# Kernel optimization log

Hardware: AMD Instinct MI355X
Metric: run time of the kernel (lower is better)

The kernel has to match this reference:

```python
import jax, jax.numpy as jnp
import numpy as np
from jax import lax

EPS_LN = 1e-5
EPS_NORM = 1e-12

def conv1x1(x, w):
    # x: [b,c,h,w], w: [o,c]
    return jnp.einsum('oc,bchw->bohw', w, x)

def dwconv3x3(x, w):
    # depthwise 3x3, w: [c,1,3,3]
    return lax.conv_general_dilated(
        x, w, window_strides=(1, 1), padding=[(1, 1), (1, 1)],
        feature_group_count=x.shape[1],
        dimension_numbers=('NCHW', 'OIHW', 'NCHW'))

def layernorm_chan(x, w, b):
    # WithBias LayerNorm over channel dim of NCHW (torch does it in b,(hw),c layout)
    mu = jnp.mean(x, axis=1, keepdims=True)
    var = jnp.mean((x - mu) ** 2, axis=1, keepdims=True)
    xn = (x - mu) / jnp.sqrt(var + EPS_LN)
    return xn * w[None, :, None, None] + b[None, :, None, None]

def l2norm(x):
    n = jnp.sqrt(jnp.sum(x * x, axis=-1, keepdims=True))
    return x / jnp.maximum(n, EPS_NORM)

def setup_inputs() -> dict:
    key = jax.random.key(0)
    ks = jax.random.split(key, 8)
    dim, heads, hidden = 64, 2, 170
    b, h, w = 2, 256, 256
    s = 0.05
    return {
        'x': jax.random.normal(ks[0], (b, dim, h, w), jnp.float32),
        'ln1_w': jnp.ones((dim,), jnp.float32),
        'ln1_b': jnp.zeros((dim,), jnp.float32),
        'w_qkv': jax.random.normal(ks[1], (dim * 3, dim), jnp.float32) * s,
        'dw_qkv': jax.random.normal(ks[2], (dim * 3, 1, 3, 3), jnp.float32) * s,
        'temperature': jnp.ones((heads, 1, 1), jnp.float32),
        'w_po': jax.random.normal(ks[3], (dim, dim), jnp.float32) * s,
        'ln2_w': jnp.ones((dim,), jnp.float32),
        'ln2_b': jnp.zeros((dim,), jnp.float32),
        'w_in': jax.random.normal(ks[4], (hidden * 2, dim), jnp.float32) * s,
        'dw_ffn': jax.random.normal(ks[5], (hidden * 2, 1, 3, 3), jnp.float32) * s,
        'w_out': jax.random.normal(ks[6], (dim, hidden), jnp.float32) * s,
    }

def attention(x, w_qkv, dw_qkv, temperature, w_po, num_heads):
    b, c, h, w = x.shape
    qkv = dwconv3x3(conv1x1(x, w_qkv), dw_qkv)            # [b,3c,h,w]
    q, k, v = jnp.split(qkv, 3, axis=1)
    def heads(t):
        return t.reshape(b, num_heads, c // num_heads, h * w)  # [b,hd,ch,hw]
    q, k, v = heads(q), heads(k), heads(v)
    q = l2norm(q)
    k = l2norm(k)
    attn = jnp.einsum('bhcs,bhds->bhcd', q, k) * temperature[None]  # [b,hd,ch,ch]
    attn = jax.nn.softmax(attn, axis=-1)
    out = jnp.einsum('bhcd,bhds->bhcs', attn, v)
    out = out.reshape(b, c, h, w)
    return conv1x1(out, w_po)

def gdfn(x, w_in, dw_ffn, w_out):
    x = dwconv3x3(conv1x1(x, w_in), dw_ffn)
    x1, x2 = jnp.split(x, 2, axis=1)
    return conv1x1(jax.nn.gelu(x1, approximate=False) * x2, w_out)

def reference(x, ln1_w, ln1_b, w_qkv, dw_qkv, temperature, w_po,
              ln2_w, ln2_b, w_in, dw_ffn, w_out):
    num_heads = temperature.shape[0]
    x = x + attention(layernorm_chan(x, ln1_w, ln1_b), w_qkv, dw_qkv,
                      temperature, w_po, num_heads)
    x = x + gdfn(layernorm_chan(x, ln2_w, ln2_b), w_in, dw_ffn, w_out)
    return x
```

## Files before the change

kernel.cpp:

```cpp
#include <hip/hip_runtime.h>
#include <math.h>

#define HW 65536

typedef __attribute__((ext_vector_type(8))) short short8;
typedef __attribute__((ext_vector_type(4))) float floatx4;
typedef __attribute__((ext_vector_type(4))) unsigned short ushortx4;

__device__ __forceinline__ float bf2f(unsigned short u){
  unsigned v = ((unsigned)u)<<16; float f; __builtin_memcpy(&f,&v,4); return f;
}
__device__ __forceinline__ unsigned short f2bf(float f){
  unsigned u; __builtin_memcpy(&u,&f,4);
  u += 0x7fffu + ((u>>16)&1u);
  return (unsigned short)(u>>16);
}
__device__ __forceinline__ int is_f32(const void* magic){
  return ((const unsigned*)magic)[0] == 0x3F800000u;
}
__device__ __forceinline__ float ldv(const void* p, size_t i, int f32){
  return f32 ? ((const float*)p)[i] : bf2f(((const unsigned short*)p)[i]);
}

__global__ __launch_bounds__(64) void k_fold(const void* __restrict__ w_qkv,
                       const void* __restrict__ ln1_w,
                       const void* __restrict__ ln1_b,
                       const void* __restrict__ w_in,
                       const void* __restrict__ ln2_w,
                       const void* __restrict__ ln2_b,
                       const void* __restrict__ w_out,
                       unsigned short* __restrict__ A1, float* __restrict__ a1, float* __restrict__ b1,
                       unsigned short* __restrict__ A5, float* __restrict__ a5, float* __restrict__ b5,
                       unsigned short* __restrict__ A7){
  int f32 = is_f32(ln1_w);
  int bid = blockIdx.x; int c = threadIdx.x;
  if (bid < 192){
    int j = bid;
    float wv = ldv(w_qkv, j*64+c, f32);
    unsigned short q = f2bf(wv*ldv(ln1_w,c,f32));
    A1[j*64+c] = q;
    float sa = bf2f(q);
    float sb = wv*ldv(ln1_b,c,f32);
    #pragma unroll
    for(int o=1;o<64;o<<=1){ sa += __shfl_xor(sa,o,64); sb += __shfl_xor(sb,o,64); }
    if (c==0){ a1[j]=sa; b1[j]=sb; }
  } else if (bid < 576){
    int j = bid-192;
    float wv = (j<340)? ldv(w_in, j*64+c, f32) : 0.f;
    unsigned short q = f2bf(wv*ldv(ln2_w,c,f32));
    A5[j*64+c]=q;
    float sa = bf2f(q);
    float sb = wv*ldv(ln2_b,c,f32);
    #pragma unroll
    for(int o=1;o<64;o<<=1){ sa += __shfl_xor(sa,o,64); sb += __shfl_xor(sb,o,64); }
    if (c==0){ a5[j]=sa; b5[j]=sb; }
  } else {
    int j = bid-576;
    #pragma unroll
    for(int t=0;t<3;t++){
      int k=t*64+c;
      A7[j*192+k] = (k<170)? f2bf(ldv(w_out, j*170+k, f32)) : (unsigned short)0;
    }
  }
}

#define BTT_STR 72
template<int F32>
__device__ __forceinline__ void gemm_ln_body(
    const unsigned short* __restrict__ A, const void* __restrict__ Bv,
    const float* __restrict__ arow, const float* __restrict__ brow,
    unsigned short* __restrict__ out, int outC, int jmax, int ntiles)
{
  __shared__ unsigned short btt[64*BTT_STR];
  __shared__ float muL[64];
  __shared__ float rsL[64];
  int tid=threadIdx.x; int w=tid>>6, lane=tid&63, m=lane&15, quad=lane>>4;
  int sblk = blockIdx.x*64; int b=sblk>>16, s=sblk&65535;
  {
    int ch = lane, px0 = w*16;
    size_t src = (size_t)b*64*HW + (size_t)ch*HW + s + px0;
    unsigned short tmp[16];
    if (F32){
      const float* sp = (const float*)Bv + src;
      #pragma unroll
      for(int q4=0;q4<4;q4++){
        floatx4 fv = *(const floatx4*)(sp + q4*4);
        #pragma unroll
        for(int k=0;k<4;k++) tmp[q4*4+k] = f2bf(fv[k]);
      }
    } else {
      const unsigned short* sp = (const unsigned short*)Bv + src;
      short8 r0 = *(const short8*)sp;
      short8 r1 = *(const short8*)(sp+8);
      #pragma unroll
      for(int jj=0;jj<8;jj++){ tmp[jj]=(unsigned short)r0[jj]; tmp[8+jj]=(unsigned short)r1[jj]; }
    }
    #pragma unroll
    for(int jj=0;jj<16;jj++) btt[(px0+jj)*BTT_STR + ch] = tmp[jj];
  }
  __syncthreads();
  short8 bfr[4][2];
  #pragma unroll
  for(int st4=0; st4<4; st4++){
    const unsigned short* row = btt + (st4*16+m)*BTT_STR + quad*8;
    short8 v0 = *(const short8*)row;
    short8 v1 = *(const short8*)(row+32);
    bfr[st4][0]=v0; bfr[st4][1]=v1;
    float sm=0.f, sq=0.f;
    #pragma unroll
    for(int jj=0;jj<8;jj++){
      float a=bf2f((unsigned short)v0[jj]); sm+=a; sq+=a*a;
      float c=bf2f((unsigned short)v1[jj]); sm+=c; sq+=c*c;
    }
    sm += __shfl_xor(sm,16,64); sq += __shfl_xor(sq,16,64);
    sm += __shfl_xor(sm,32,64); sq += __shfl_xor(sq,32,64);
    float m_ = sm*(1.f/64.f);
    float var = sq*(1.f/64.f) - m_*m_;
    if (w==0 && quad==0){ muL[st4*16+m]=m_; rsL[st4*16+m]=1.f/sqrtf(var+1e-5f); }
  }
  __syncthreads();
  for(int jt=w; jt<ntiles; jt+=4){
    int j = jt*16 + m;
    const unsigned short* ap = A + j*64 + quad*8;
    short8 af0 = *(const short8*)ap;
    short8 af1 = *(const short8*)(ap+32);
    float aj = arow[j], bj = brow[j];
    unsigned short* op = out + ((size_t)b*outC + j)*HW + s;
    bool ok = (j < jmax);
    #pragma unroll
    for(int st4=0; st4<4; st4++){
      floatx4 acc = {0.f,0.f,0.f,0.f};
      acc = __builtin_amdgcn_mfma_f32_16x16x32_bf16(bfr[st4][0], af0, acc, 0,0,0);
      acc = __builtin_amdgcn_mfma_f32_16x16x32_bf16(bfr[st4][1], af1, acc, 0,0,0);
      floatx4 m4 = *(const floatx4*)(muL + st4*16 + quad*4);
      floatx4 r4 = *(const floatx4*)(rsL + st4*16 + quad*4);
      ushortx4 pk;
      #pragma unroll
      for(int r=0;r<4;r++) pk[r] = f2bf(r4[r]*(acc[r] - m4[r]*aj) + bj);
      if (ok) *(ushortx4*)(op + st4*16 + quad*4) = pk;
    }
  }
}
__global__ __launch_bounds__(256) void k_gemm_ln(
    const unsigned short* __restrict__ A, const void* __restrict__ B,
    const float* __restrict__ arow, const float* __restrict__ brow,
    unsigned short* __restrict__ out,
    int outC, int jmax, int ntiles, const void* __restrict__ magic, int mode)
{
  int f32 = (mode==1) ? 1 : (mode==2 ? 0 : is_f32(magic));
  if (f32) gemm_ln_body<1>(A,B,arow,brow,out,outC,jmax,ntiles);
  else     gemm_ln_body<0>(A,B,arow,brow,out,outC,jmax,ntiles);
}

#define GTT_STR 200
__global__ __launch_bounds__(256) void k_gemm_out(
    const unsigned short* __restrict__ A7, const unsigned short* __restrict__ G,
    const unsigned short* __restrict__ xmid, void* __restrict__ outp, const void* __restrict__ magic)
{
  __shared__ unsigned short gtt[64*GTT_STR];
  int f32 = is_f32(magic);
  int tid=threadIdx.x; int w=tid>>6, lane=tid&63, m=lane&15, quad=lane>>4;
  int sblk = blockIdx.x*64; int b=sblk>>16, s=sblk&65535;
  const unsigned short* Gb = G + (size_t)b*170*HW + s;
  {
    int px0 = w*16;
    #pragma unroll
    for(int rep=0; rep<3; rep++){
      int ch = rep*64 + lane;
      const unsigned short* sp = Gb + (size_t)ch*HW + px0;
      short8 r0 = *(const short8*)sp;
      short8 r1 = *(const short8*)(sp+8);
      #pragma unroll
      for(int jj=0;jj<8;jj++){
        gtt[(px0+jj)*GTT_STR + ch]   = (unsigned short)r0[jj];
        gtt[(px0+8+jj)*GTT_STR + ch] = (unsigned short)r1[jj];
      }
    }
  }
  __syncthreads();
  int j = w*16 + m;
  const unsigned short* ap = A7 + j*192 + quad*8;
  short8 af[6];
  #pragma unroll
  for(int ks=0;ks<6;ks++) af[ks] = *(const short8*)(ap + ks*32);
  #pragma unroll
  for(int st4=0; st4<4; st4++){
    const unsigned short* row = gtt + (st4*16+m)*GTT_STR + quad*8;
    floatx4 acc = {0.f,0.f,0.f,0.f};
    #pragma unroll
    for(int ks=0;ks<6;ks++){
      short8 bf = *(const short8*)(row + ks*32);
      acc = __builtin_amdgcn_mfma_f32_16x16x32_bf16(bf, af[ks], acc, 0,0,0);
    }
    size_t idx0 = ((size_t)b*64 + j)*HW + s + st4*16 + quad*4;
    ushortx4 xm4 = *(const ushortx4*)(xmid + idx0);
    if (f32){
      floatx4 o;
      #pragma unroll
      for(int r=0;r<4;r++) o[r] = acc[r] + bf2f(xm4[r]);
      *(floatx4*)((float*)outp + idx0) = o;
    } else {
      ushortx4 o;
      #pragma unroll
      for(int r=0;r<4;r++) o[r] = f2bf(acc[r] + bf2f(xm4[r]));
      *(ushortx4*)((unsigned short*)outp + idx0) = o;
    }
  }
}

__device__ __forceinline__ void load_row(const unsigned short* __restrict__ sp,
    int y, int x0, int oct, float* __restrict__ f){
  if((unsigned)y < 256u){
    const unsigned short* p = sp + y*256 + x0;
    short8 v = *(const short8*)p;
    #pragma unroll
    for(int k=0;k<8;k++) f[k+1] = bf2f((unsigned short)v[k]);
    f[0] = oct      ? bf2f(p[-1]) : 0.f;
    f[9] = (oct<31) ? bf2f(p[8])  : 0.f;
  } else {
    #pragma unroll
    for(int k=0;k<10;k++) f[k] = 0.f;
  }
}

__device__ __forceinline__ void conv_row(const float* __restrict__ r0,
    const float* __restrict__ r1, const float* __restrict__ r2,
    const float* __restrict__ w, float* __restrict__ o){
  #pragma unroll
  for(int k=0;k<8;k++){
    o[k] = w[0]*r0[k] + w[1]*r0[k+1] + w[2]*r0[k+2]
         + w[3]*r1[k] + w[4]*r1[k+1] + w[5]*r1[k+2]
         + w[6]*r2[k] + w[7]*r2[k+1] + w[8]*r2[k+2];
  }
}

__global__ __launch_bounds__(256) void k_dwconv(const unsigned short* __restrict__ src,
    const void* __restrict__ wdw, unsigned short* __restrict__ dst, int C,
    const void* __restrict__ magic){
  int f32 = is_f32(magic);
  int tid=threadIdx.x;
  int bc = blockIdx.y;
  int ch = bc % C;
  int oct = tid&31, strip = tid>>5;
  int x0 = oct*8;
  int y0 = blockIdx.x*64 + strip*8;
  const unsigned short* sp = src + (size_t)bc*HW;
  float w9[9];
  #pragma unroll
  for(int i=0;i<9;i++) w9[i]=ldv(wdw, ch*9+i, f32);
  unsigned short* dp = dst + (size_t)bc*HW + (size_t)y0*256 + x0;
  float A[10],B[10],C_[10],D[10];
  load_row(sp, y0-1, x0, oct, A);
  load_row(sp, y0,   x0, oct, B);
  load_row(sp, y0+1, x0, oct, C_);
  int y = y0;
#define DSTEP(P,Q,R,S) { \
    load_row(sp, y+2, x0, oct, S); \
    float o8[8]; \
    conv_row(P,Q,R, w9, o8); \
    short8 st; \
    _Pragma("unroll") \
    for(int k=0;k<8;k++) st[k]=(short)f2bf(o8[k]); \
    *(short8*)dp = st; dp += 256; y++; }
  for(int t=0;t<2;t++){
    DSTEP(A,B,C_,D)
    DSTEP(B,C_,D,A)
    DSTEP(C_,D,A,B)
    DSTEP(D,A,B,C_)
  }
#undef DSTEP
}

__global__ __launch_bounds__(256) void k_ffn_dw(const unsigned short* __restrict__ src,
    const void* __restrict__ wdw, unsigned short* __restrict__ g,
    const void* __restrict__ magic){
  int f32 = is_f32(magic);
  int tid=threadIdx.x;
  int bi = blockIdx.y;
  int b = bi/170, i = bi - b*170;
  int oct = tid&31, strip = tid>>5;
  int x0 = oct*8;
  int y0 = blockIdx.x*64 + strip*8;
  const unsigned short* s1 = src + ((size_t)b*340 + i)*HW;
  const unsigned short* s2 = src + ((size_t)b*340 + 170 + i)*HW;
  float wa[9], wb[9];
  #pragma unroll
  for(int q=0;q<9;q++){ wa[q]=ldv(wdw, i*9+q, f32); wb[q]=ldv(wdw, (i+170)*9+q, f32); }
  unsigned short* gp = g + ((size_t)b*170 + i)*HW + (size_t)y0*256 + x0;
  float A1[10],B1[10],C1[10],D1[10];
  float A2[10],B2[10],C2[10],D2[10];
  load_row(s1, y0-1, x0, oct, A1); load_row(s2, y0-1, x0, oct, A2);
  load_row(s1, y0,   x0, oct, B1); load_row(s2, y0,   x0, oct, B2);
  load_row(s1, y0+1, x0, oct, C1); load_row(s2, y0+1, x0, oct, C2);
  int y = y0;
#define FSTEP(P,Q,R,S) { \
    load_row(s1, y+2, x0, oct, S##1); \
    load_row(s2, y+2, x0, oct, S##2); \
    float oa[8], oc[8]; \
    conv_row(P##1,Q##1,R##1, wa, oa); \
    conv_row(P##2,Q##2,R##2, wb, oc); \
    short8 st; \
    _Pragma("unroll") \
    for(int k=0;k<8;k++){ \
      float u = oa[k]*(1.59576912f + 0.07135481f*oa[k]*oa[k]); \
      float ge = oa[k]/(1.f + __expf(-u)); \
      st[k]=(short)f2bf(ge*oc[k]); \
    } \
    *(short8*)gp = st; gp += 256; y++; }
  for(int t=0;t<2;t++){
    FSTEP(A,B,C,D)
    FSTEP(B,C,D,A)
    FSTEP(C,D,A,B)
    FSTEP(D,A,B,C)
  }
#undef FSTEP
}

__global__ __launch_bounds__(256) void k_attn_qk(const unsigned short* __restrict__ qkv,
    float* __restrict__ S, float* __restrict__ qn, float* __restrict__ kn){
  int tid=threadIdx.x; int w=tid>>6, lane=tid&63, m=lane&15, quad=lane>>4;
  int ct=w>>1, dt=w&1;
  int bh=blockIdx.y; int b=bh>>1, hd=bh&1;
  int p0 = blockIdx.x*512;
  const unsigned short* qrow = qkv + ((size_t)(b*192 + hd*32 + ct*16 + m))*HW + p0 + quad*8;
  const unsigned short* krow = qkv + ((size_t)(b*192 + 64 + hd*32 + dt*16 + m))*HW + p0 + quad*8;
  floatx4 acc = {0.f,0.f,0.f,0.f};
  float nq=0.f, nk=0.f;
  for(int it=0; it<16; it++){
    short8 a = *(const short8*)(qrow + it*32);
    short8 bq = *(const short8*)(krow + it*32);
    if (dt==0){
      #pragma unroll
      for(int jj=0;jj<8;jj++){ float v=bf2f((unsigned short)a[jj]); nq+=v*v; }
    }
    if (ct==0){
      #pragma unroll
      for(int jj=0;jj<8;jj++){ float v=bf2f((unsigned short)bq[jj]); nk+=v*v; }
    }
    acc = __builtin_amdgcn_mfma_f32_16x16x32_bf16(a, bq, acc, 0,0,0);
  }
  nq += __shfl_xor(nq,16,64); nq += __shfl_xor(nq,32,64);
  nk += __shfl_xor(nk,16,64); nk += __shfl_xor(nk,32,64);
  if (dt==0 && quad==0) atomicAdd(&qn[bh*32 + ct*16 + m], nq);
  if (ct==0 && quad==0) atomicAdd(&kn[bh*32 + dt*16 + m], nk);
  #pragma unroll
  for(int r=0;r<4;r++)
    atomicAdd(&S[(bh*32 + ct*16 + quad*4 + r)*32 + dt*16 + m], acc[r]);
}

__global__ void k_attn_fin(const float* __restrict__ S, const float* __restrict__ qn,
    const float* __restrict__ kn, const void* __restrict__ temp,
    const void* __restrict__ w_po, unsigned short* __restrict__ Mbf,
    const void* __restrict__ magic){
  int f32 = is_f32(magic);
  __shared__ float attn[2][32][32];
  __shared__ float invq[64], invk[64];
  int b = blockIdx.x; int tid=threadIdx.x;
  if (tid<64){
    int bh=b*2+(tid>>5); int c=tid&31;
    invq[tid] = 1.f/fmaxf(sqrtf(qn[bh*32+c]),1e-12f);
    invk[tid] = 1.f/fmaxf(sqrtf(kn[bh*32+c]),1e-12f);
  }
  __syncthreads();
  if (tid<64){
    int hd=tid>>5, c=tid&31; int bh=b*2+hd;
    float tmp = ldv(temp, hd, f32);
    float row[32]; float mx=-1e30f;
    for(int d=0;d<32;d++){
      float v = S[(bh*32+c)*32+d]*invq[tid]*invk[hd*32+d]*tmp;
      row[d]=v; mx=fmaxf(mx,v);
    }
    float sum=0.f;
    for(int d=0;d<32;d++){ row[d]=expf(row[d]-mx); sum+=row[d]; }
    float inv=1.f/sum;
    for(int d=0;d<32;d++) attn[hd][c][d]=row[d]*inv;
  }
  __syncthreads();
  for(int idx=tid; idx<4096; idx+=256){
    int o=idx>>6, d=idx&63; int hd=d>>5, dd=d&31;
    float sacc=0.f;
    for(int c=0;c<32;c++) sacc += ldv(w_po, o*64 + hd*32 + c, f32) * attn[hd][c][dd];
    Mbf[(size_t)b*4096 + o*64 + d] = f2bf(sacc);
  }
}

#define XSTR 72
__global__ __launch_bounds__(256) void k_attn_ffn(const void* __restrict__ x,
    const unsigned short* __restrict__ qkv, const unsigned short* __restrict__ Mbf,
    unsigned short* __restrict__ xmid,
    const unsigned short* __restrict__ A5, const float* __restrict__ a5, const float* __restrict__ b5,
    unsigned short* __restrict__ ffn_pre, const void* __restrict__ magic){
  __shared__ unsigned short vtt[64*XSTR];
  __shared__ unsigned short xt[64*XSTR];
  __shared__ float muL[64];
  __shared__ float rsL[64];
  int f32 = is_f32(magic);
  int tid=threadIdx.x; int w=tid>>6, lane=tid&63, m=lane&15, quad=lane>>4;
  int sblk = blockIdx.x*64; int b=sblk>>16, s=sblk&65535;
  const unsigned short* vp = qkv + ((size_t)(b*192 + 128))*HW + s;
  {
    int ch = lane, px0 = w*16;
    const unsigned short* sp = vp + (size_t)ch*HW + px0;
    short8 r0 = *(const short8*)sp;
    short8 r1 = *(const short8*)(sp+8);
    #pragma unroll
    for(int jj=0;jj<8;jj++){
      vtt[(px0+jj)*XSTR + ch]   = (unsigned short)r0[jj];
      vtt[(px0+8+jj)*XSTR + ch] = (unsigned short)r1[jj];
    }
  }
  int jme = w*16 + m;
  const unsigned short* ap = Mbf + (size_t)b*4096 + jme*64 + quad*8;
  short8 af0 = *(const short8*)ap;
  short8 af1 = *(const short8*)(ap+32);
  __syncthreads();
  short8 bfr[4][2];
  #pragma unroll
  for(int st4=0; st4<4; st4++){
    const unsigned short* row = vtt + (st4*16+m)*XSTR + quad*8;
    bfr[st4][0] = *(const short8*)row;
    bfr[st4][1] = *(const short8*)(row+32);
  }
  size_t xbase = (size_t)b*64*HW + s;
  #pragma unroll
  for(int st4=0; st4<4; st4++){
    floatx4 acc = {0.f,0.f,0.f,0.f};
    acc = __builtin_amdgcn_mfma_f32_16x16x32_bf16(bfr[st4][0], af0, acc, 0,0,0);
    acc = __builtin_amdgcn_mfma_f32_16x16x32_bf16(bfr[st4][1], af1, acc, 0,0,0);
    size_t idx0 = xbase + (size_t)jme*HW + st4*16 + quad*4;
    ushortx4 h;
    if (f32){
      floatx4 x4 = *(const floatx4*)((const float*)x + idx0);
      #pragma unroll
      for(int r=0;r<4;r++) h[r] = f2bf(acc[r] + x4[r]);
    } else {
      ushortx4 x4 = *(const ushortx4*)((const unsigned short*)x + idx0);
      #pragma unroll
      for(int r=0;r<4;r++) h[r] = f2bf(acc[r] + bf2f(x4[r]));
    }
    *(ushortx4*)(xmid + idx0) = h;
    #pragma unroll
    for(int r=0;r<4;r++) xt[(st4*16+quad*4+r)*XSTR + jme] = h[r];
  }
  __syncthreads();
  #pragma unroll
  for(int st4=0; st4<4; st4++){
    const unsigned short* row = xt + (st4*16+m)*XSTR + quad*8;
    short8 v0 = *(const short8*)row;
    short8 v1 = *(const short8*)(row+32);
    bfr[st4][0]=v0; bfr[st4][1]=v1;
    float sm=0.f, sq=0.f;
    #pragma unroll
    for(int jj=0;jj<8;jj++){
      float a=bf2f((unsigned short)v0[jj]); sm+=a; sq+=a*a;
      float c=bf2f((unsigned short)v1[jj]); sm+=c; sq+=c*c;
    }
    sm += __shfl_xor(sm,16,64); sq += __shfl_xor(sq,16,64);
    sm += __shfl_xor(sm,32,64); sq += __shfl_xor(sq,32,64);
    float m_ = sm*(1.f/64.f);
    float var = sq*(1.f/64.f) - m_*m_;
    if (w==0 && quad==0){ muL[st4*16+m]=m_; rsL[st4*16+m]=1.f/sqrtf(var+1e-5f); }
  }
  __syncthreads();
  for(int jt=w; jt<24; jt+=4){
    int j = jt*16 + m;
    const unsigned short* a5p = A5 + j*64 + quad*8;
    short8 g0 = *(const short8*)a5p;
    short8 g1 = *(const short8*)(a5p+32);
    float aj = a5[j], bj = b5[j];
    unsigned short* op = ffn_pre + ((size_t)b*340 + j)*HW + s;
    bool ok = (j < 340);
    #pragma unroll
    for(int st4=0; st4<4; st4++){
      floatx4 acc = {0.f,0.f,0.f,0.f};
      acc = __builtin_amdgcn_mfma_f32_16x16x32_bf16(bfr[st4][0], g0, acc, 0,0,0);
      acc = __builtin_amdgcn_mfma_f32_16x16x32_bf16(bfr[st4][1], g1, acc, 0,0,0);
      floatx4 m4 = *(const floatx4*)(muL + st4*16 + quad*4);
      floatx4 r4 = *(const floatx4*)(rsL + st4*16 + quad*4);
      ushortx4 pk;
      #pragma unroll
      for(int r=0;r<4;r++) pk[r] = f2bf(r4[r]*(acc[r] - m4[r]*aj) + bj);
      if (ok) *(ushortx4*)(op + st4*16 + quad*4) = pk;
    }
  }
}

extern "C" void kernel_launch(void* const* d_in, const int* in_sizes, int n_in,
                              void* d_out, int out_size, void* d_ws, size_t ws_size,
                              hipStream_t stream){
  (void)in_sizes; (void)n_in; (void)out_size; (void)ws_size;
  const void* x     = d_in[0];
  const void* ln1_w = d_in[1];
  const void* ln1_b = d_in[2];
  const void* w_qkv = d_in[3];
  const void* dw_qkv= d_in[4];
  const void* temp  = d_in[5];
  const void* w_po  = d_in[6];
  const void* ln2_w = d_in[7];
  const void* ln2_b = d_in[8];
  const void* w_in  = d_in[9];
  const void* dw_ffn= d_in[10];
  const void* w_out = d_in[11];

  char* ws = (char*)d_ws;
  size_t off = 0;
  auto alloc = [&](size_t n)->void*{ void* p = ws + off; off = (off + n + 255) & ~(size_t)255; return p; };

  unsigned short* A1 = (unsigned short*)alloc(192*64*2);
  float* a1 = (float*)alloc(192*4);
  float* b1 = (float*)alloc(192*4);
  unsigned short* A5 = (unsigned short*)alloc(384*64*2);
  float* a5 = (float*)alloc(384*4);
  float* b5 = (float*)alloc(384*4);
  unsigned short* A7 = (unsigned short*)alloc(64*192*2);
  float* S  = (float*)alloc(4*32*32*4);
  float* qn = (float*)alloc(128*4);
  float* kn = (float*)alloc(128*4);
  unsigned short* Mbf = (unsigned short*)alloc(2*64*64*2);
  unsigned short* xmid = (unsigned short*)alloc((size_t)2*64*HW*2);
  unsigned short* regionA = (unsigned short*)alloc((size_t)2*340*HW*2);
  unsigned short* regionB = (unsigned short*)alloc((size_t)2*192*HW*2);

  k_fold<<<dim3(640), dim3(64), 0, stream>>>(w_qkv, ln1_w, ln1_b, w_in, ln2_w, ln2_b, w_out,
                                             A1, a1, b1, A5, a5, b5, A7);

  k_gemm_ln<<<dim3(2048), dim3(256), 0, stream>>>(A1, x, a1, b1, regionA, 192, 192, 12, ln1_w, 0);
  k_dwconv<<<dim3(4,384), dim3(256), 0, stream>>>(regionA, dw_qkv, regionB, 192, ln1_w);

  hipMemsetAsync(S, 0, 16384+512+512, stream);
  k_attn_qk<<<dim3(128,4), dim3(256), 0, stream>>>(regionB, S, qn, kn);
  k_attn_fin<<<dim3(2), dim3(256), 0, stream>>>(S, qn, kn, temp, w_po, Mbf, ln1_w);

  k_attn_ffn<<<dim3(2048), dim3(256), 0, stream>>>(x, regionB, Mbf, xmid,
                                                   A5, a5, b5, regionA, ln1_w);
  k_ffn_dw<<<dim3(4,340), dim3(256), 0, stream>>>(regionA, dw_ffn, regionB, ln1_w);
  k_gemm_out<<<dim3(2048), dim3(256), 0, stream>>>(A7, regionB, xmid, d_out, ln1_w);
}
```

Measured before the change: 306.1 us.

## Preload all conv rows up front and use lane shuffles for halo pixels

After: 279.4 us. 8.7% less time.

```diff
diff --git a/kernel.cpp b/kernel.cpp
--- a/kernel.cpp
+++ b/kernel.cpp
@@ -208,21 +208,6 @@
   }
 }
 
-__device__ __forceinline__ void load_row(const unsigned short* __restrict__ sp,
-    int y, int x0, int oct, float* __restrict__ f){
-  if((unsigned)y < 256u){
-    const unsigned short* p = sp + y*256 + x0;
-    short8 v = *(const short8*)p;
-    #pragma unroll
-    for(int k=0;k<8;k++) f[k+1] = bf2f((unsigned short)v[k]);
-    f[0] = oct      ? bf2f(p[-1]) : 0.f;
-    f[9] = (oct<31) ? bf2f(p[8])  : 0.f;
-  } else {
-    #pragma unroll
-    for(int k=0;k<10;k++) f[k] = 0.f;
-  }
-}
-
 __device__ __forceinline__ void conv_row(const float* __restrict__ r0,
     const float* __restrict__ r1, const float* __restrict__ r2,
     const float* __restrict__ w, float* __restrict__ o){
@@ -234,40 +219,55 @@
   }
 }
 
-__global__ __launch_bounds__(256) void k_dwconv(const unsigned short* __restrict__ src,
+#define CVT(F, V) { \
+    int lv = __shfl((int)(unsigned short)(V)[7], lane-1, 64); \
+    int rv = __shfl((int)(unsigned short)(V)[0], lane+1, 64); \
+    F[0] = oct       ? bf2f((unsigned short)lv) : 0.f; \
+    F[9] = (oct<31)  ? bf2f((unsigned short)rv) : 0.f; \
+    _Pragma("unroll") \
+    for(int k=0;k<8;k++) F[k+1] = bf2f((unsigned short)(V)[k]); \
+  }
+
+__global__ __launch_bounds__(256,4) void k_dwconv(const unsigned short* __restrict__ src,
     const void* __restrict__ wdw, unsigned short* __restrict__ dst, int C,
     const void* __restrict__ magic){
   int f32 = is_f32(magic);
   int tid=threadIdx.x;
   int bc = blockIdx.y;
   int ch = bc % C;
+  int lane = tid&63;
   int oct = tid&31, strip = tid>>5;
   int x0 = oct*8;
   int y0 = blockIdx.x*64 + strip*8;
   const unsigned short* sp = src + (size_t)bc*HW;
+  short8 R[10];
+  #pragma unroll
+  for(int r=0;r<10;r++){
+    int y = y0-1+r;
+    if((unsigned)y<256u) R[r] = *(const short8*)(sp + y*256 + x0);
+    else { short8 z = {0,0,0,0,0,0,0,0}; R[r] = z; }
+  }
   float w9[9];
   #pragma unroll
   for(int i=0;i<9;i++) w9[i]=ldv(wdw, ch*9+i, f32);
   unsigned short* dp = dst + (size_t)bc*HW + (size_t)y0*256 + x0;
   float A[10],B[10],C_[10],D[10];
-  load_row(sp, y0-1, x0, oct, A);
-  load_row(sp, y0,   x0, oct, B);
-  load_row(sp, y0+1, x0, oct, C_);
-  int y = y0;
-#define DSTEP(P,Q,R,S) { \
-    load_row(sp, y+2, x0, oct, S); \
+  CVT(A, R[0]) CVT(B, R[1]) CVT(C_, R[2])
+#define DSTEP(P,Q,Rr) { \
     float o8[8]; \
-    conv_row(P,Q,R, w9, o8); \
+    conv_row(P,Q,Rr, w9, o8); \
     short8 st; \
     _Pragma("unroll") \
     for(int k=0;k<8;k++) st[k]=(short)f2bf(o8[k]); \
-    *(short8*)dp = st; dp += 256; y++; }
-  for(int t=0;t<2;t++){
-    DSTEP(A,B,C_,D)
-    DSTEP(B,C_,D,A)
-    DSTEP(C_,D,A,B)
-    DSTEP(D,A,B,C_)
-  }
+    *(short8*)dp = st; dp += 256; }
+  DSTEP(A,B,C_)  CVT(D, R[3])
+  DSTEP(B,C_,D)  CVT(A, R[4])
+  DSTEP(C_,D,A)  CVT(B, R[5])
+  DSTEP(D,A,B)   CVT(C_,R[6])
+  DSTEP(A,B,C_)  CVT(D, R[7])
+  DSTEP(B,C_,D)  CVT(A, R[8])
+  DSTEP(C_,D,A)  CVT(B, R[9])
+  DSTEP(D,A,B)
 #undef DSTEP
 }
 
@@ -278,27 +278,37 @@
   int tid=threadIdx.x;
   int bi = blockIdx.y;
   int b = bi/170, i = bi - b*170;
+  int lane = tid&63;
   int oct = tid&31, strip = tid>>5;
   int x0 = oct*8;
   int y0 = blockIdx.x*64 + strip*8;
   const unsigned short* s1 = src + ((size_t)b*340 + i)*HW;
   const unsigned short* s2 = src + ((size_t)b*340 + 170 + i)*HW;
+  short8 R1[10], R2[10];
+  #pragma unroll
+  for(int r=0;r<10;r++){
+    int y = y0-1+r;
+    if((unsigned)y<256u){
+      int o = y*256 + x0;
+      R1[r] = *(const short8*)(s1 + o);
+      R2[r] = *(const short8*)(s2 + o);
+    } else {
+      short8 z = {0,0,0,0,0,0,0,0}; R1[r] = z; R2[r] = z;
+    }
+  }
   float wa[9], wb[9];
   #pragma unroll
   for(int q=0;q<9;q++){ wa[q]=ldv(wdw, i*9+q, f32); wb[q]=ldv(wdw, (i+170)*9+q, f32); }
   unsigned short* gp = g + ((size_t)b*170 + i)*HW + (size_t)y0*256 + x0;
   float A1[10],B1[10],C1[10],D1[10];
   float A2[10],B2[10],C2[10],D2[10];
-  load_row(s1, y0-1, x0, oct, A1); load_row(s2, y0-1, x0, oct, A2);
-  load_row(s1, y0,   x0, oct, B1); load_row(s2, y0,   x0, oct, B2);
-  load_row(s1, y0+1, x0, oct, C1); load_row(s2, y0+1, x0, oct, C2);
-  int y = y0;
-#define FSTEP(P,Q,R,S) { \
-    load_row(s1, y+2, x0, oct, S##1); \
-    load_row(s2, y+2, x0, oct, S##2); \
+  CVT(A1, R1[0]) CVT(B1, R1[1]) CVT(C1, R1[2])
+  CVT(A2, R2[0]) CVT(B2, R2[1]) CVT(C2, R2[2])
+#define CVT2(S, ri) CVT(S##1, R1[ri]) CVT(S##2, R2[ri])
+#define FSTEP(P,Q,Rr) { \
     float oa[8], oc[8]; \
-    conv_row(P##1,Q##1,R##1, wa, oa); \
-    conv_row(P##2,Q##2,R##2, wb, oc); \
+    conv_row(P##1,Q##1,Rr##1, wa, oa); \
+    conv_row(P##2,Q##2,Rr##2, wb, oc); \
     short8 st; \
     _Pragma("unroll") \
     for(int k=0;k<8;k++){ \
@@ -306,14 +316,17 @@
       float ge = oa[k]/(1.f + __expf(-u)); \
       st[k]=(short)f2bf(ge*oc[k]); \
     } \
-    *(short8*)gp = st; gp += 256; y++; }
-  for(int t=0;t<2;t++){
-    FSTEP(A,B,C,D)
-    FSTEP(B,C,D,A)
-    FSTEP(C,D,A,B)
-    FSTEP(D,A,B,C)
-  }
+    *(short8*)gp = st; gp += 256; }
+  FSTEP(A,B,C)  CVT2(D,3)
+  FSTEP(B,C,D)  CVT2(A,4)
+  FSTEP(C,D,A)  CVT2(B,5)
+  FSTEP(D,A,B)  CVT2(C,6)
+  FSTEP(A,B,C)  CVT2(D,7)
+  FSTEP(B,C,D)  CVT2(A,8)
+  FSTEP(C,D,A)  CVT2(B,9)
+  FSTEP(D,A,B)
 #undef FSTEP
+#undef CVT2
 }
 
 __global__ __launch_bounds__(256) void k_attn_qk(const unsigned short* __restrict__ qkv,
```
